# Performance work log

Measured on AMD Instinct MI355X. Metric: run time of the kernel, lower is better.

Reference implementation:

```python
import jax, jax.numpy as jnp
import numpy as np

K = 3          # spline order
NUM = 32       # grid intervals G
IN_DIM = 256
OUT_DIM = 512
BATCH = 2048


def _b_spline_basis(x, grid, k):
    """Cox-de-Boor recursion. x: (B, I); grid: (I, G+2k+1) -> (B, I, G+k)."""
    xg = x[:, :, None]                      # (B, I, 1)
    g = grid[None, :, :]                    # (1, I, G+2k+1)
    val = ((xg >= g[:, :, :-1]) & (xg < g[:, :, 1:])).astype(x.dtype)
    for p in range(1, k + 1):
        left = (xg - g[:, :, :-(p + 1)]) / (g[:, :, p:-1] - g[:, :, :-(p + 1)])
        right = (g[:, :, p + 1:] - xg) / (g[:, :, p + 1:] - g[:, :, 1:-p])
        val = left * val[:, :, :-1] + right * val[:, :, 1:]
    return val                               # (B, I, G+k)


def setup_inputs() -> dict:
    key = jax.random.key(0)
    k1, k2, k3 = jax.random.split(key, 3)
    x = jax.random.normal(k1, (BATCH, IN_DIM), dtype=jnp.float32)
    # uniform grid on [-1, 1], extended by k knots on each side (extend_grid)
    base = np.linspace(-1.0, 1.0, NUM + 1)
    h = 2.0 / NUM
    ext = np.concatenate([base[0] - h * np.arange(K, 0, -1), base,
                          base[-1] + h * np.arange(1, K + 1)]).astype(np.float32)
    grid = jnp.tile(jnp.asarray(ext)[None, :], (IN_DIM, 1))  # (I, G+2k+1)
    coef = 0.1 * jax.random.normal(k2, (IN_DIM, OUT_DIM, NUM + K), dtype=jnp.float32)
    scale_base = jax.random.normal(k3, (IN_DIM, OUT_DIM), dtype=jnp.float32) / np.sqrt(IN_DIM).astype(np.float32)
    scale_sp = jnp.ones((IN_DIM, OUT_DIM), dtype=jnp.float32) / np.sqrt(IN_DIM).astype(np.float32)
    mask = jnp.ones((IN_DIM, OUT_DIM), dtype=jnp.float32)
    return {"x": x, "grid": grid, "coef": coef,
            "scale_base": scale_base, "scale_sp": scale_sp, "mask": mask}


def reference(x, grid, coef, scale_base, scale_sp, mask):
    base = jax.nn.silu(x)                                   # b(x) residual, (B, I)
    bases = _b_spline_basis(x, grid, K)                     # (B, I, G+k)
    # coef2curve: einsum('ijk,jlk->ijl') in pykan -> (B, I, O)
    y = jnp.einsum('bik,iok->bio', bases, coef)
    y = scale_base[None, :, :] * base[:, :, None] + scale_sp[None, :, :] * y
    y = mask[None, :, :] * y
    return jnp.sum(y, axis=1)                               # (B, O)
```

## Files before the change

### kernel.cpp

```cpp
#include <hip/hip_runtime.h>
#include <math.h>

#define BATCH   2048
#define IN_DIM  256
#define OUT_DIM 512
#define NK      35
#define KS      48
#define BTILE   128
#define OTILE   128
#define ICHUNK  32
#define NSPLIT  8
#define COEFS_BYTES ((size_t)IN_DIM * OUT_DIM * KS * 2)
#define PART_ELEMS  ((size_t)BATCH * OUT_DIM)

__device__ __forceinline__ unsigned short f2bf(float x) {
    unsigned u = __float_as_uint(x);
    u += 0x7FFF + ((u >> 16) & 1);
    return (unsigned short)(u >> 16);
}
__device__ __forceinline__ float bf2f(unsigned short h) {
    return __uint_as_float(((unsigned)h) << 16);
}
__device__ __forceinline__ unsigned pack2(unsigned short a, unsigned short b) {
    return (unsigned)a | ((unsigned)b << 16);
}

typedef __bf16 bf16x8 __attribute__((ext_vector_type(8)));
typedef float  f32x16 __attribute__((ext_vector_type(16)));
typedef unsigned int u32;

__device__ __forceinline__ void gload_lds16(const void* g, void* l) {
    __builtin_amdgcn_global_load_lds((const __attribute__((address_space(1))) u32*)g,
                                     (__attribute__((address_space(3))) u32*)l, 16, 0, 0);
}

#define PR 32
__global__ __launch_bounds__(256) void kan_prep(
    const float* __restrict__ coef,
    const float* __restrict__ scale_base,
    const float* __restrict__ scale_sp,
    const float* __restrict__ mask,
    unsigned short* __restrict__ coefS)
{
    __shared__ float sc[PR * NK];
    __shared__ float sspm[PR], ssbm[PR];
    const int t    = threadIdx.x;
    const int row0 = blockIdx.x * PR;

    {
        const float4* csrc = (const float4*)(coef + (size_t)row0 * NK);
        float4* cdst = (float4*)sc;
        cdst[t] = csrc[t];
        if (t < 24) cdst[t + 256] = csrc[t + 256];
    }
    if (t < PR) {
        float m = mask[row0 + t];
        sspm[t] = scale_sp[row0 + t] * m;
        ssbm[t] = scale_base[row0 + t] * m;
    }
    __syncthreads();

    if (t < PR * 6) {
        int r = t / 6;
        int q = t - r * 6;
        float spm = sspm[r];
        const float* c = sc + r * NK;
        uint4 v = make_uint4(0u, 0u, 0u, 0u);
        if (q < 4) {
            const float* cq = c + q * 8;
            v.x = pack2(f2bf(cq[0] * spm), f2bf(cq[1] * spm));
            v.y = pack2(f2bf(cq[2] * spm), f2bf(cq[3] * spm));
            v.z = pack2(f2bf(cq[4] * spm), f2bf(cq[5] * spm));
            v.w = pack2(f2bf(cq[6] * spm), f2bf(cq[7] * spm));
        } else if (q == 4) {
            float sbm = ssbm[r];
            unsigned short hi = f2bf(sbm);
            unsigned short lo = f2bf(sbm - bf2f(hi));
            v.x = pack2(f2bf(c[32] * spm), f2bf(c[33] * spm));
            v.y = pack2(f2bf(c[34] * spm), 0);
            v.z = pack2(hi, hi);
            v.w = pack2(lo, 0);
        }
        ((uint4*)coefS)[(size_t)(row0 + r) * 6 + q] = v;
    }
}

__global__ __launch_bounds__(320, 2) void kan_mfma(
    const float* __restrict__ x,
    const unsigned short* __restrict__ coefS,
    float* __restrict__ part)
{
    __shared__ __align__(16) short sA[2 * BTILE * KS];
    __shared__ __align__(16) short sB[2 * OTILE * KS];

    const int t    = threadIdx.x;
    const int lane = t & 63;
    const int l31  = lane & 31, lh = lane >> 5;
    const int o0   = blockIdx.x * OTILE;
    const int b0   = blockIdx.y * BTILE;
    const int ic0  = blockIdx.z * ICHUNK;
    const bool prod = (t >= 256);
    const int w    = t >> 6;
    const int wr   = w & 1;
    const int wc   = w >> 1;

    {
        uint4 z = make_uint4(0, 0, 0, 0);
        #pragma unroll
        for (int u = 0; u < 5; ++u) {
            int idx = t + 320 * u;
            if (idx < (2 * BTILE * KS * 2) / 16) ((uint4*)sA)[idx] = z;
        }
    }

    f32x16 acc00 = {}, acc01 = {}, acc10 = {}, acc11 = {};

    float xp0 = 0.f, xp1 = 0.f;
    int ojb[2][2] = {{0, 0}, {0, 0}};

    auto stageA = [&](short* arow, float xv, int& ojbn) {
        arow[ojbn] = 0; arow[ojbn + 1] = 0; arow[ojbn + 2] = 0; arow[ojbn + 3] = 0;
        float xn = (xv + 1.1875f) * 16.0f;
        float jf = floorf(xn);
        int   j  = (int)jf;
        float u  = xn - jf;
        bool valid = (xn >= 0.0f) && (j <= 37);
        float u2 = u * u, u3 = u2 * u;
        float w0 = (1.0f / 6.0f) * (1.0f - 3.0f * u + 3.0f * u2 - u3);
        float w1 = (1.0f / 6.0f) * (3.0f * u3 - 6.0f * u2 + 4.0f);
        float w2 = (1.0f / 6.0f) * (-3.0f * u3 + 3.0f * u2 + 3.0f * u + 1.0f);
        float w3 = (1.0f / 6.0f) * u3;
        int jb = j - 3;
        if (valid) {
            if ((unsigned)jb       < 35u) arow[jb]     = f2bf(w0);
            if ((unsigned)(jb + 1) < 35u) arow[jb + 1] = f2bf(w1);
            if ((unsigned)(jb + 2) < 35u) arow[jb + 2] = f2bf(w2);
            if ((unsigned)(jb + 3) < 35u) arow[jb + 3] = f2bf(w3);
        }
        ojbn = min(max(jb, 0), 31);
        float sig = 1.0f / (1.0f + __expf(-xv));
        float s   = xv * sig;
        unsigned short shi = f2bf(s);
        unsigned short slo = f2bf(s - bf2f(shi));
        *(unsigned int*)(arow + 36) = pack2(shi, slo);
        arow[38] = shi;
    };

    auto issueB = [&](int i, int buf) {
        const char* gsrc = (const char*)(coefS + ((size_t)i * OUT_DIM + o0) * KS);
        #pragma unroll
        for (int q = 0; q < 12; ++q) {
            gload_lds16(gsrc + (size_t)(q * 64 + lane) * 16,
                        (void*)(sB + buf * (OTILE * KS) + q * 512));
        }
    };

    __syncthreads();

    if (prod) {
        issueB(ic0, 0);
        xp0 = x[(size_t)(b0 + lane) * IN_DIM + ic0];
        xp1 = x[(size_t)(b0 + lane + 64) * IN_DIM + ic0];
        stageA(sA + lane * KS, xp0, ojb[0][0]);
        stageA(sA + (lane + 64) * KS, xp1, ojb[0][1]);
        xp0 = x[(size_t)(b0 + lane) * IN_DIM + ic0 + 1];
        xp1 = x[(size_t)(b0 + lane + 64) * IN_DIM + ic0 + 1];
    }
    __syncthreads();

    auto body = [&](int it, int cur, int nxt) {
        if (prod) {
            if (it + 1 < ICHUNK) {
                issueB(ic0 + it + 1, nxt);
                stageA(sA + nxt * (BTILE * KS) + lane * KS, xp0, ojb[nxt][0]);
                stageA(sA + nxt * (BTILE * KS) + (lane + 64) * KS, xp1, ojb[nxt][1]);
                if (it + 2 < ICHUNK) {
                    xp0 = x[(size_t)(b0 + lane) * IN_DIM + ic0 + it + 2];
                    xp1 = x[(size_t)(b0 + lane + 64) * IN_DIM + ic0 + it + 2];
                }
            }
        } else {
            const short* Ab = sA + cur * (BTILE * KS) + (wr * 64 + l31) * KS + lh * 8;
            const short* Bb = sB + cur * (OTILE * KS) + (wc * 64 + l31) * KS + lh * 8;
            #pragma unroll
            for (int s = 0; s < 3; ++s) {
                bf16x8 a0 = *(const bf16x8*)(Ab + s * 16);
                bf16x8 a1 = *(const bf16x8*)(Ab + 32 * KS + s * 16);
                bf16x8 b0 = *(const bf16x8*)(Bb + s * 16);
                bf16x8 b1 = *(const bf16x8*)(Bb + 32 * KS + s * 16);
                acc00 = __builtin_amdgcn_mfma_f32_32x32x16_bf16(a0, b0, acc00, 0, 0, 0);
                acc01 = __builtin_amdgcn_mfma_f32_32x32x16_bf16(a0, b1, acc01, 0, 0, 0);
                acc10 = __builtin_amdgcn_mfma_f32_32x32x16_bf16(a1, b0, acc10, 0, 0, 0);
                acc11 = __builtin_amdgcn_mfma_f32_32x32x16_bf16(a1, b1, acc11, 0, 0, 0);
            }
        }
        __syncthreads();
    };

    #pragma unroll 2
    for (int it = 0; it < ICHUNK; ++it) body(it, it & 1, (it + 1) & 1);

    if (!prod) {
        float* tp = (float*)sA + w * (32 * 36);
        float* pdst = part + (size_t)blockIdx.z * PART_ELEMS;
        #pragma unroll
        for (int r = 0; r < 2; ++r) {
            #pragma unroll
            for (int c = 0; c < 2; ++c) {
                const f32x16& acc = (r == 0) ? ((c == 0) ? acc00 : acc01)
                                             : ((c == 0) ? acc10 : acc11);
                #pragma unroll
                for (int reg = 0; reg < 16; ++reg) {
                    int row = (reg & 3) + 8 * (reg >> 2) + 4 * lh;
                    tp[row * 36 + l31] = acc[reg];
                }
                int cc = (lane & 7) * 4;
                #pragma unroll
                for (int j = 0; j < 4; ++j) {
                    int rr = j * 8 + (lane >> 3);
                    float4 v = *(float4*)&tp[rr * 36 + cc];
                    int rowg = b0 + wr * 64 + r * 32 + rr;
                    int colg = o0 + wc * 64 + c * 32 + cc;
                    *(float4*)&pdst[(size_t)rowg * OUT_DIM + colg] = v;
                }
            }
        }
    }
}

__global__ __launch_bounds__(256) void kan_reduce(
    const float4* __restrict__ part, float4* __restrict__ out)
{
    const size_t e = (size_t)blockIdx.x * 256 + threadIdx.x;
    float4 s = part[e];
    #pragma unroll
    for (int z = 1; z < NSPLIT; ++z) {
        float4 v = part[(size_t)z * (PART_ELEMS / 4) + e];
        s.x += v.x; s.y += v.y; s.z += v.z; s.w += v.w;
    }
    out[e] = s;
}

extern "C" void kernel_launch(void* const* d_in, const int* in_sizes, int n_in,
                              void* d_out, int out_size, void* d_ws, size_t ws_size,
                              hipStream_t stream) {
    const float* x          = (const float*)d_in[0];
    const float* coef       = (const float*)d_in[2];
    const float* scale_base = (const float*)d_in[3];
    const float* scale_sp   = (const float*)d_in[4];
    const float* mask       = (const float*)d_in[5];
    unsigned short* coefS   = (unsigned short*)d_ws;
    float* part             = (float*)((char*)d_ws + COEFS_BYTES);

    kan_prep<<<dim3(IN_DIM * OUT_DIM / PR), dim3(256), 0, stream>>>(
        coef, scale_base, scale_sp, mask, coefS);
    kan_mfma<<<dim3(OUT_DIM / OTILE, BATCH / BTILE, NSPLIT), dim3(320), 0, stream>>>(
        x, coefS, part);
    kan_reduce<<<dim3(BATCH * OUT_DIM / 4 / 256), dim3(256), 0, stream>>>(
        (const float4*)part, (float4*)d_out);
}
```

Measured before the change: 125.4 us.

## Precompute spline basis rows in separate kernel and stream them via async LDS loads

Moves the B-spline basis and SiLU evaluation out of the MFMA kernel's producer warp into a new prep kernel that writes a bf16 basis matrix (IN_DIM x BATCH x 48) to workspace. The MFMA kernel's producer now only issues async global-to-LDS loads for both A and B tiles, removing per-iteration ALU work and the strided x loads from the critical path. In exchange, each basis row is computed once rather than once per output tile, but this adds an extra launch and roughly 50 MB of workspace traffic that is written and then read back, with A-tile global bandwidth replacing the cheap x reads.

```diff
diff --git a/kernel.cpp b/kernel.cpp
--- a/kernel.cpp
+++ b/kernel.cpp
@@ -11,6 +11,7 @@
 #define ICHUNK  32
 #define NSPLIT  8
 #define COEFS_BYTES ((size_t)IN_DIM * OUT_DIM * KS * 2)
+#define AX_BYTES    ((size_t)IN_DIM * BATCH * KS * 2)
 #define PART_ELEMS  ((size_t)BATCH * OUT_DIM)
 
 __device__ __forceinline__ unsigned short f2bf(float x) {
@@ -85,8 +86,55 @@
     }
 }
 
+__global__ __launch_bounds__(256) void kan_prepA(
+    const float* __restrict__ x,
+    unsigned short* __restrict__ Ax)
+{
+    __shared__ __align__(16) short sr[256 * KS];
+    const int t  = threadIdx.x;
+    const int i  = blockIdx.x >> 3;
+    const int b0 = (blockIdx.x & 7) * 256;
+
+    float xv = x[(size_t)(b0 + t) * IN_DIM + i];
+
+    short* arow = sr + t * KS;
+    {
+        uint4 z = make_uint4(0, 0, 0, 0);
+        #pragma unroll
+        for (int q = 0; q < 6; ++q) ((uint4*)arow)[q] = z;
+    }
+    float xn = (xv + 1.1875f) * 16.0f;
+    float jf = floorf(xn);
+    int   j  = (int)jf;
+    float u  = xn - jf;
+    bool valid = (xn >= 0.0f) && (j <= 37);
+    float u2 = u * u, u3 = u2 * u;
+    float w0 = (1.0f / 6.0f) * (1.0f - 3.0f * u + 3.0f * u2 - u3);
+    float w1 = (1.0f / 6.0f) * (3.0f * u3 - 6.0f * u2 + 4.0f);
+    float w2 = (1.0f / 6.0f) * (-3.0f * u3 + 3.0f * u2 + 3.0f * u + 1.0f);
+    float w3 = (1.0f / 6.0f) * u3;
+    int jb = j - 3;
+    if (valid) {
+        if ((unsigned)jb       < 35u) arow[jb]     = f2bf(w0);
+        if ((unsigned)(jb + 1) < 35u) arow[jb + 1] = f2bf(w1);
+        if ((unsigned)(jb + 2) < 35u) arow[jb + 2] = f2bf(w2);
+        if ((unsigned)(jb + 3) < 35u) arow[jb + 3] = f2bf(w3);
+    }
+    float sig = 1.0f / (1.0f + __expf(-xv));
+    float s   = xv * sig;
+    unsigned short shi = f2bf(s);
+    unsigned short slo = f2bf(s - bf2f(shi));
+    *(unsigned int*)(arow + 36) = pack2(shi, slo);
+    arow[38] = shi;
+    __syncthreads();
+
+    uint4* dst = (uint4*)(Ax + ((size_t)i * BATCH + b0) * KS);
+    #pragma unroll
+    for (int q = 0; q < 6; ++q) dst[t + 256 * q] = ((uint4*)sr)[t + 256 * q];
+}
+
 __global__ __launch_bounds__(320, 2) void kan_mfma(
-    const float* __restrict__ x,
+    const unsigned short* __restrict__ Ax,
     const unsigned short* __restrict__ coefS,
     float* __restrict__ part)
 {
@@ -104,81 +152,29 @@
     const int wr   = w & 1;
     const int wc   = w >> 1;
 
-    {
-        uint4 z = make_uint4(0, 0, 0, 0);
-        #pragma unroll
-        for (int u = 0; u < 5; ++u) {
-            int idx = t + 320 * u;
-            if (idx < (2 * BTILE * KS * 2) / 16) ((uint4*)sA)[idx] = z;
-        }
-    }
-
     f32x16 acc00 = {}, acc01 = {}, acc10 = {}, acc11 = {};
 
-    float xp0 = 0.f, xp1 = 0.f;
-    int ojb[2][2] = {{0, 0}, {0, 0}};
-
-    auto stageA = [&](short* arow, float xv, int& ojbn) {
-        arow[ojbn] = 0; arow[ojbn + 1] = 0; arow[ojbn + 2] = 0; arow[ojbn + 3] = 0;
-        float xn = (xv + 1.1875f) * 16.0f;
-        float jf = floorf(xn);
-        int   j  = (int)jf;
-        float u  = xn - jf;
-        bool valid = (xn >= 0.0f) && (j <= 37);
-        float u2 = u * u, u3 = u2 * u;
-        float w0 = (1.0f / 6.0f) * (1.0f - 3.0f * u + 3.0f * u2 - u3);
-        float w1 = (1.0f / 6.0f) * (3.0f * u3 - 6.0f * u2 + 4.0f);
-        float w2 = (1.0f / 6.0f) * (-3.0f * u3 + 3.0f * u2 + 3.0f * u + 1.0f);
-        float w3 = (1.0f / 6.0f) * u3;
-        int jb = j - 3;
-        if (valid) {
-            if ((unsigned)jb       < 35u) arow[jb]     = f2bf(w0);
-            if ((unsigned)(jb + 1) < 35u) arow[jb + 1] = f2bf(w1);
-            if ((unsigned)(jb + 2) < 35u) arow[jb + 2] = f2bf(w2);
-            if ((unsigned)(jb + 3) < 35u) arow[jb + 3] = f2bf(w3);
-        }
-        ojbn = min(max(jb, 0), 31);
-        float sig = 1.0f / (1.0f + __expf(-xv));
-        float s   = xv * sig;
-        unsigned short shi = f2bf(s);
-        unsigned short slo = f2bf(s - bf2f(shi));
-        *(unsigned int*)(arow + 36) = pack2(shi, slo);
-        arow[38] = shi;
+    auto issueAB = [&](int i, int buf) {
+        const char* ga = (const char*)(Ax + ((size_t)i * BATCH + b0) * KS);
+        const char* gb = (const char*)(coefS + ((size_t)i * OUT_DIM + o0) * KS);
+        #pragma unroll
+        for (int q = 0; q < 12; ++q) {
+            gload_lds16(ga + (size_t)(q * 64 + lane) * 16,
+                        (void*)(sA + buf * (BTILE * KS) + q * 512));
+        }
+        #pragma unroll
+        for (int q = 0; q < 12; ++q) {
+            gload_lds16(gb + (size_t)(q * 64 + lane) * 16,
+                        (void*)(sB + buf * (OTILE * KS) + q * 512));
+        }
     };
 
-    auto issueB = [&](int i, int buf) {
-        const char* gsrc = (const char*)(coefS + ((size_t)i * OUT_DIM + o0) * KS);
-        #pragma unroll
-        for (int q = 0; q < 12; ++q) {
-            gload_lds16(gsrc + (size_t)(q * 64 + lane) * 16,
-                        (void*)(sB + buf * (OTILE * KS) + q * 512));
-        }
-    };
-
-    __syncthreads();
-
-    if (prod) {
-        issueB(ic0, 0);
-        xp0 = x[(size_t)(b0 + lane) * IN_DIM + ic0];
-        xp1 = x[(size_t)(b0 + lane + 64) * IN_DIM + ic0];
-        stageA(sA + lane * KS, xp0, ojb[0][0]);
-        stageA(sA + (lane + 64) * KS, xp1, ojb[0][1]);
-        xp0 = x[(size_t)(b0 + lane) * IN_DIM + ic0 + 1];
-        xp1 = x[(size_t)(b0 + lane + 64) * IN_DIM + ic0 + 1];
-    }
+    if (prod) issueAB(ic0, 0);
     __syncthreads();
 
     auto body = [&](int it, int cur, int nxt) {
         if (prod) {
-            if (it + 1 < ICHUNK) {
-                issueB(ic0 + it + 1, nxt);
-                stageA(sA + nxt * (BTILE * KS) + lane * KS, xp0, ojb[nxt][0]);
-                stageA(sA + nxt * (BTILE * KS) + (lane + 64) * KS, xp1, ojb[nxt][1]);
-                if (it + 2 < ICHUNK) {
-                    xp0 = x[(size_t)(b0 + lane) * IN_DIM + ic0 + it + 2];
-                    xp1 = x[(size_t)(b0 + lane + 64) * IN_DIM + ic0 + it + 2];
-                }
-            }
+            if (it + 1 < ICHUNK) issueAB(ic0 + it + 1, nxt);
         } else {
             const short* Ab = sA + cur * (BTILE * KS) + (wr * 64 + l31) * KS + lh * 8;
             const short* Bb = sB + cur * (OTILE * KS) + (wc * 64 + l31) * KS + lh * 8;
@@ -250,12 +246,14 @@
     const float* scale_sp   = (const float*)d_in[4];
     const float* mask       = (const float*)d_in[5];
     unsigned short* coefS   = (unsigned short*)d_ws;
-    float* part             = (float*)((char*)d_ws + COEFS_BYTES);
+    unsigned short* Ax      = (unsigned short*)((char*)d_ws + COEFS_BYTES);
+    float* part             = (float*)((char*)d_ws + COEFS_BYTES + AX_BYTES);
 
     kan_prep<<<dim3(IN_DIM * OUT_DIM / PR), dim3(256), 0, stream>>>(
         coef, scale_base, scale_sp, mask, coefS);
+    kan_prepA<<<dim3(IN_DIM * 8), dim3(256), 0, stream>>>(x, Ax);
     kan_mfma<<<dim3(OUT_DIM / OTILE, BATCH / BTILE, NSPLIT), dim3(320), 0, stream>>>(
-        x, coefS, part);
+        Ax, coefS, part);
     kan_reduce<<<dim3(BATCH * OUT_DIM / 4 / 256), dim3(256), 0, stream>>>(
         (const float4*)part, (float4*)d_out);
 }
```

Result: slower. 147.3 us (+17.5%).

## Widen producer to four waves with register-staged B prefetch

Applied to the files above, without the earlier changes.

The block grows from 320 to 512 threads, so 256 producer threads stage A and B in place of one wave. B tiles now go through registers, loaded two iterations ahead and then written to LDS, replacing the direct global-to-LDS loads. Each A row is split between two threads that zero and fill halves of the row, which removes the earlier full-buffer zeroing and the tracking of old offsets. The goal is to shorten the producer critical path per iteration, at the cost of more registers, higher occupancy demands and an extra pass through VGPRs.

```diff
diff --git a/kernel.cpp b/kernel.cpp
--- a/kernel.cpp
+++ b/kernel.cpp
@@ -27,12 +27,6 @@
 
 typedef __bf16 bf16x8 __attribute__((ext_vector_type(8)));
 typedef float  f32x16 __attribute__((ext_vector_type(16)));
-typedef unsigned int u32;
-
-__device__ __forceinline__ void gload_lds16(const void* g, void* l) {
-    __builtin_amdgcn_global_load_lds((const __attribute__((address_space(1))) u32*)g,
-                                     (__attribute__((address_space(3))) u32*)l, 16, 0, 0);
-}
 
 #define PR 32
 __global__ __launch_bounds__(256) void kan_prep(
@@ -85,7 +79,7 @@
     }
 }
 
-__global__ __launch_bounds__(320, 2) void kan_mfma(
+__global__ __launch_bounds__(512, 4) void kan_mfma(
     const float* __restrict__ x,
     const unsigned short* __restrict__ coefS,
     float* __restrict__ part)
@@ -104,22 +98,32 @@
     const int wr   = w & 1;
     const int wc   = w >> 1;
 
-    {
-        uint4 z = make_uint4(0, 0, 0, 0);
-        #pragma unroll
-        for (int u = 0; u < 5; ++u) {
-            int idx = t + 320 * u;
-            if (idx < (2 * BTILE * KS * 2) / 16) ((uint4*)sA)[idx] = z;
-        }
-    }
-
     f32x16 acc00 = {}, acc01 = {}, acc10 = {}, acc11 = {};
 
-    float xp0 = 0.f, xp1 = 0.f;
-    int ojb[2][2] = {{0, 0}, {0, 0}};
-
-    auto stageA = [&](short* arow, float xv, int& ojbn) {
-        arow[ojbn] = 0; arow[ojbn + 1] = 0; arow[ojbn + 2] = 0; arow[ojbn + 3] = 0;
+    const int p = t - 256;
+    const int r = p >> 1;
+    const int h = p & 1;
+    uint4 rb[2][3];
+    float xf[2];
+
+    auto loadB = [&](int i, int s) {
+        const uint4* gb = (const uint4*)(coefS + ((size_t)i * OUT_DIM + o0) * KS);
+        rb[s][0] = gb[p];
+        rb[s][1] = gb[p + 256];
+        rb[s][2] = gb[p + 512];
+    };
+    auto writeB = [&](int buf, int s) {
+        uint4* db = (uint4*)(sB + buf * (OTILE * KS));
+        db[p]       = rb[s][0];
+        db[p + 256] = rb[s][1];
+        db[p + 512] = rb[s][2];
+    };
+    auto stageA = [&](int buf, float xv) {
+        short* arow = sA + buf * (BTILE * KS) + r * KS + h * 24;
+        uint4 z = make_uint4(0u, 0u, 0u, 0u);
+        ((uint4*)arow)[0] = z;
+        ((uint4*)arow)[1] = z;
+        ((uint4*)arow)[2] = z;
         float xn = (xv + 1.1875f) * 16.0f;
         float jf = floorf(xn);
         int   j  = (int)jf;
@@ -132,52 +136,46 @@
         float w3 = (1.0f / 6.0f) * u3;
         int jb = j - 3;
         if (valid) {
-            if ((unsigned)jb       < 35u) arow[jb]     = f2bf(w0);
-            if ((unsigned)(jb + 1) < 35u) arow[jb + 1] = f2bf(w1);
-            if ((unsigned)(jb + 2) < 35u) arow[jb + 2] = f2bf(w2);
-            if ((unsigned)(jb + 3) < 35u) arow[jb + 3] = f2bf(w3);
-        }
-        ojbn = min(max(jb, 0), 31);
-        float sig = 1.0f / (1.0f + __expf(-xv));
-        float s   = xv * sig;
-        unsigned short shi = f2bf(s);
-        unsigned short slo = f2bf(s - bf2f(shi));
-        *(unsigned int*)(arow + 36) = pack2(shi, slo);
-        arow[38] = shi;
+            float ws[4] = {w0, w1, w2, w3};
+            #pragma unroll
+            for (int q = 0; q < 4; ++q) {
+                int slot = jb + q;
+                int loc  = slot - h * 24;
+                if ((unsigned)slot < 35u && (unsigned)loc < 24u)
+                    arow[loc] = f2bf(ws[q]);
+            }
+        }
+        if (h) {
+            float sig = 1.0f / (1.0f + __expf(-xv));
+            float s   = xv * sig;
+            unsigned short shi = f2bf(s);
+            unsigned short slo = f2bf(s - bf2f(shi));
+            *(unsigned int*)(arow + 12) = pack2(shi, slo);
+            arow[14] = shi;
+        }
     };
 
-    auto issueB = [&](int i, int buf) {
-        const char* gsrc = (const char*)(coefS + ((size_t)i * OUT_DIM + o0) * KS);
-        #pragma unroll
-        for (int q = 0; q < 12; ++q) {
-            gload_lds16(gsrc + (size_t)(q * 64 + lane) * 16,
-                        (void*)(sB + buf * (OTILE * KS) + q * 512));
-        }
-    };
-
+    if (prod) {
+        loadB(ic0, 0);
+        xf[0] = x[(size_t)(b0 + r) * IN_DIM + ic0];
+        writeB(0, 0);
+        stageA(0, xf[0]);
+        loadB(ic0 + 1, 1);
+        xf[1] = x[(size_t)(b0 + r) * IN_DIM + ic0 + 1];
+    }
     __syncthreads();
 
-    if (prod) {
-        issueB(ic0, 0);
-        xp0 = x[(size_t)(b0 + lane) * IN_DIM + ic0];
-        xp1 = x[(size_t)(b0 + lane + 64) * IN_DIM + ic0];
-        stageA(sA + lane * KS, xp0, ojb[0][0]);
-        stageA(sA + (lane + 64) * KS, xp1, ojb[0][1]);
-        xp0 = x[(size_t)(b0 + lane) * IN_DIM + ic0 + 1];
-        xp1 = x[(size_t)(b0 + lane + 64) * IN_DIM + ic0 + 1];
-    }
-    __syncthreads();
-
-    auto body = [&](int it, int cur, int nxt) {
+    #pragma unroll 2
+    for (int it = 0; it < ICHUNK; ++it) {
+        const int cur = it & 1, nxt = cur ^ 1;
         if (prod) {
             if (it + 1 < ICHUNK) {
-                issueB(ic0 + it + 1, nxt);
-                stageA(sA + nxt * (BTILE * KS) + lane * KS, xp0, ojb[nxt][0]);
-                stageA(sA + nxt * (BTILE * KS) + (lane + 64) * KS, xp1, ojb[nxt][1]);
-                if (it + 2 < ICHUNK) {
-                    xp0 = x[(size_t)(b0 + lane) * IN_DIM + ic0 + it + 2];
-                    xp1 = x[(size_t)(b0 + lane + 64) * IN_DIM + ic0 + it + 2];
-                }
+                writeB(nxt, nxt);
+                stageA(nxt, xf[nxt]);
+            }
+            if (it + 2 < ICHUNK) {
+                loadB(ic0 + it + 2, cur);
+                xf[cur] = x[(size_t)(b0 + r) * IN_DIM + ic0 + it + 2];
             }
         } else {
             const short* Ab = sA + cur * (BTILE * KS) + (wr * 64 + l31) * KS + lh * 8;
@@ -195,20 +193,17 @@
             }
         }
         __syncthreads();
-    };
-
-    #pragma unroll 2
-    for (int it = 0; it < ICHUNK; ++it) body(it, it & 1, (it + 1) & 1);
+    }
 
     if (!prod) {
         float* tp = (float*)sA + w * (32 * 36);
         float* pdst = part + (size_t)blockIdx.z * PART_ELEMS;
         #pragma unroll
-        for (int r = 0; r < 2; ++r) {
+        for (int rr2 = 0; rr2 < 2; ++rr2) {
             #pragma unroll
             for (int c = 0; c < 2; ++c) {
-                const f32x16& acc = (r == 0) ? ((c == 0) ? acc00 : acc01)
-                                             : ((c == 0) ? acc10 : acc11);
+                const f32x16& acc = (rr2 == 0) ? ((c == 0) ? acc00 : acc01)
+                                               : ((c == 0) ? acc10 : acc11);
                 #pragma unroll
                 for (int reg = 0; reg < 16; ++reg) {
                     int row = (reg & 3) + 8 * (reg >> 2) + 4 * lh;
@@ -219,7 +214,7 @@
                 for (int j = 0; j < 4; ++j) {
                     int rr = j * 8 + (lane >> 3);
                     float4 v = *(float4*)&tp[rr * 36 + cc];
-                    int rowg = b0 + wr * 64 + r * 32 + rr;
+                    int rowg = b0 + wr * 64 + rr2 * 32 + rr;
                     int colg = o0 + wc * 64 + c * 32 + cc;
                     *(float4*)&pdst[(size_t)rowg * OUT_DIM + colg] = v;
                 }
@@ -254,7 +249,7 @@
 
     kan_prep<<<dim3(IN_DIM * OUT_DIM / PR), dim3(256), 0, stream>>>(
         coef, scale_base, scale_sp, mask, coefS);
-    kan_mfma<<<dim3(OUT_DIM / OTILE, BATCH / BTILE, NSPLIT), dim3(320), 0, stream>>>(
+    kan_mfma<<<dim3(OUT_DIM / OTILE, BATCH / BTILE, NSPLIT), dim3(512), 0, stream>>>(
         x, coefS, part);
     kan_reduce<<<dim3(BATCH * OUT_DIM / 4 / 256), dim3(256), 0, stream>>>(
         (const float4*)part, (float4*)d_out);
```

After: 157.2 us. +25.4%, slower.
